# Kernel tuning notes

Hardware: AMD Instinct MI355X
Metric: run time of the kernel (lower is better)

The kernel has to match this reference:

```python
import jax, jax.numpy as jnp
import numpy as np

N_EMBED = 8192
EMBED_DIM = 64
BETA = 0.25


def setup_inputs() -> dict:
    key = jax.random.key(0)
    k_z, k_e = jax.random.split(key)
    z = jax.random.normal(k_z, (16, 4096, EMBED_DIM), dtype=jnp.float32)
    # embedding.weight.data.uniform_(-1/n_embed, 1/n_embed)
    embedding = jax.random.uniform(
        k_e, (N_EMBED, EMBED_DIM), dtype=jnp.float32,
        minval=-1.0 / N_EMBED, maxval=1.0 / N_EMBED)
    return {"z": z, "embedding": embedding}


def reference(z, embedding):
    # z: [B, H, C] with C == embed_dim (no permute needed)
    B, H, C = z.shape
    z_flat = z.reshape(-1, C)                      # [N, C]
    # squared euclidean distances: ||z||^2 + ||e||^2 - 2 z e^T
    d = (jnp.sum(z_flat ** 2, axis=1, keepdims=True)
         + jnp.sum(embedding ** 2, axis=1)
         - 2.0 * jnp.matmul(z_flat, embedding.T))  # [N, n_embed]
    idx = jnp.argmin(d, axis=1)                    # [N]
    z_q = embedding[idx].reshape(z.shape)          # gather + reshape
    sg = jax.lax.stop_gradient
    loss = (jnp.mean((sg(z_q) - z) ** 2)
            + BETA * jnp.mean((z_q - sg(z)) ** 2))
    # straight-through estimator
    z_q = z + sg(z_q - z)
    return z_q, loss, idx.reshape(B, H)
```

## Files before the change

### kernel.cpp

```cpp
#include <hip/hip_runtime.h>

typedef __attribute__((ext_vector_type(8))) short short8;
typedef __attribute__((ext_vector_type(16))) float floatx16;
typedef unsigned int u32;
typedef unsigned short u16;
typedef unsigned long long u64;

#define NROWS 65536
#define NEMB 8192
#define DIM 64
#define LOSS_OFF ((size_t)NROWS * DIM)
#define IDX_OFF (LOSS_OFF + 1)
#define CAPQ 20
#define CSTRIDE 82
#define NPRE 2

#define WS_EFRAG_OFF 0u
#define WS_LPART_OFF (1u << 20)
#define WS_QUEUE_OFF ((1u << 20) + 8192u)
#define WS_QCNT_OFF  ((1u << 20) + 8192u + (256u << 10))
#define WS_LOVR_OFF  (WS_QCNT_OFF + 4u)
#define WS_NEED      (WS_QCNT_OFF + 64u)

__device__ __forceinline__ unsigned short f2bf(float f) {
    u32 x = __float_as_uint(f);
    return (unsigned short)((x + 0x7fffu + ((x >> 16) & 1u)) >> 16);
}

__device__ __forceinline__ float zsum_np(const float* zf) {
    float r[8];
#pragma unroll
    for (int j = 0; j < 8; ++j) r[j] = zf[j] * zf[j];
#pragma unroll
    for (int i = 8; i < 64; i += 8) {
#pragma unroll
        for (int j = 0; j < 8; ++j) r[j] += zf[i + j] * zf[i + j];
    }
    return ((r[0] + r[1]) + (r[2] + r[3])) + ((r[4] + r[5]) + (r[6] + r[7]));
}

__device__ __forceinline__ float dot_chain(const float* zf, const float* e) {
    float acc = 0.f;
#pragma unroll
    for (int i = 0; i < 16; ++i) {
        float4 ev = ((const float4*)e)[i];
        acc = fmaf(zf[4 * i + 0], ev.x, acc);
        acc = fmaf(zf[4 * i + 1], ev.y, acc);
        acc = fmaf(zf[4 * i + 2], ev.z, acc);
        acc = fmaf(zf[4 * i + 3], ev.w, acc);
    }
    return acc;
}

__device__ __forceinline__ float vmax16_3(const floatx16& a) {
    float m0 = fmaxf(fmaxf(a[0], a[1]), a[2]);
    float m1 = fmaxf(fmaxf(a[3], a[4]), a[5]);
    float m2 = fmaxf(fmaxf(a[6], a[7]), a[8]);
    float m3 = fmaxf(fmaxf(a[9], a[10]), a[11]);
    float m4 = fmaxf(fmaxf(a[12], a[13]), a[14]);
    float n0 = fmaxf(fmaxf(m0, m1), m2);
    float n1 = fmaxf(fmaxf(m3, m4), a[15]);
    return fmaxf(n0, n1);
}

extern "C" __global__ __launch_bounds__(256)
void vq_prep(const float* __restrict__ emb, u32* __restrict__ efrag,
             u32* __restrict__ qcount, float* __restrict__ loss_over) {
    int tid = blockIdx.x * 256 + threadIdx.x;
    int t = tid >> 8, kc = (tid >> 5) & 7, m = tid & 31;
    const float* e = emb + (((size_t)t * 32 + m) * 64 + kc * 8);
    float4 a = ((const float4*)e)[0];
    float4 b = ((const float4*)e)[1];
    u32 w0 = (u32)f2bf(a.x) | ((u32)f2bf(a.y) << 16);
    u32 w1 = (u32)f2bf(a.z) | ((u32)f2bf(a.w) << 16);
    u32 w2 = (u32)f2bf(b.x) | ((u32)f2bf(b.y) << 16);
    u32 w3 = (u32)f2bf(b.z) | ((u32)f2bf(b.w) << 16);
    ((uint4*)efrag)[tid] = make_uint4(w0, w1, w2, w3);
    if (tid == 0) { qcount[0] = 0u; *loss_over = 0.f; }
}

extern "C" __global__ __launch_bounds__(256, 2)
void vq_screen(const float* __restrict__ z, const u32* __restrict__ efrag,
               const float* __restrict__ emb, float* __restrict__ out,
               float* __restrict__ lpart, u32* __restrict__ queue,
               u32* __restrict__ qcount) {
    __shared__ u16 cand[128 * CSTRIDE];
    __shared__ u32 cnt_l[512];
    __shared__ float runm_sh[128][2];
    __shared__ u32 win[128];
    __shared__ float lsum[4];
    const int tid = threadIdx.x;
    const int wave = tid >> 6, lane = tid & 63;
    const int rlo = lane & 31, h = lane >> 5;
    const int rowbase = blockIdx.x * 128 + (wave >> 1) * 64;
    const int sub = (wave & 1) * 2 + h;
    const int wp = wave & 1;

    if (tid < 128) { runm_sh[tid][0] = -3.4e38f; runm_sh[tid][1] = -3.4e38f; }

    short8 zfr[2][4];
    float eps_[2];
#pragma unroll
    for (int rt = 0; rt < 2; ++rt) {
        const float* zp = z + (size_t)(rowbase + rt * 32 + rlo) * 64;
        float sa = 0.f;
#pragma unroll
        for (int s = 0; s < 4; ++s) {
            const float4* p = (const float4*)(zp + s * 16 + h * 8);
            float4 a = p[0], b = p[1];
            union { short8 v; unsigned short e[8]; } u;
            u.e[0] = f2bf(a.x); u.e[1] = f2bf(a.y);
            u.e[2] = f2bf(a.z); u.e[3] = f2bf(a.w);
            u.e[4] = f2bf(b.x); u.e[5] = f2bf(b.y);
            u.e[6] = f2bf(b.z); u.e[7] = f2bf(b.w);
            zfr[rt][s] = u.v;
            sa += fabsf(a.x) + fabsf(a.y) + fabsf(a.z) + fabsf(a.w)
                + fabsf(b.x) + fabsf(b.y) + fabsf(b.z) + fabsf(b.w);
        }
        sa += __shfl_xor(sa, 32);
        eps_[rt] = fmaf(1.1e-6f, sa, 1e-7f);
    }
    float runm[2] = { -3.4e38f, -3.4e38f };
    u32 pc[2] = { 0u, 0u };
    __syncthreads();

    const u32* fbase = efrag + wp * 4096 + (size_t)h * 128 + (size_t)rlo * 4;
    for (int ii = 0; ii < 32 + NPRE; ++ii) {
        const int t = (ii < NPRE) ? ii : (ii - NPRE);
        const u32* tb = fbase + (size_t)t * 8192;

#pragma unroll
        for (int rt = 0; rt < 2; ++rt) {
            const int rowl = (wave >> 1) * 64 + rt * 32 + rlo;
            runm[rt] = fmaxf(runm[rt], runm_sh[rowl][wp ^ 1]);
        }

        floatx16 acc[4][2];
#pragma unroll
        for (int et = 0; et < 4; ++et)
#pragma unroll
            for (int rt = 0; rt < 2; ++rt) acc[et][rt] = 0.f;

#pragma unroll
        for (int s = 0; s < 4; ++s) {
            short8 af[4];
#pragma unroll
            for (int et = 0; et < 4; ++et)
                af[et] = *(const short8*)(tb + et * 1024 + s * 256);
#pragma unroll
            for (int et = 0; et < 4; ++et)
#pragma unroll
                for (int rt = 0; rt < 2; ++rt)
                    acc[et][rt] = __builtin_amdgcn_mfma_f32_32x32x16_bf16(
                        af[et], zfr[rt][s], acc[et][rt], 0, 0, 0);
        }

#pragma unroll
        for (int rt = 0; rt < 2; ++rt) {
            const int rowl = (wave >> 1) * 64 + rt * 32 + rlo;
            float vm[4];
#pragma unroll
            for (int et = 0; et < 4; ++et) vm[et] = vmax16_3(acc[et][rt]);
            float m64 = fmaxf(fmaxf(vm[0], vm[1]), fmaxf(vm[2], vm[3]));
            runm[rt] = fmaxf(runm[rt], m64);
            runm[rt] = fmaxf(runm[rt], __shfl_xor(runm[rt], 32));
            if (ii >= NPRE) {
                const float thr = runm[rt] - eps_[rt];
                if (m64 >= thr) {
                    const int ebase = t * 256 + wp * 128;
                    const u32 cbase = (u32)rowl * CSTRIDE + (u32)sub * CAPQ;
#pragma unroll
                    for (int et = 0; et < 4; ++et) {
                        if (vm[et] >= thr) {
#pragma unroll
                            for (int r = 0; r < 16; ++r) {
                                float v = acc[et][rt][r];
                                if (v >= thr) {
                                    int j = ebase + et * 32 + ((r & 3) + 8 * (r >> 2) + 4 * h);
                                    if (pc[rt] < CAPQ) cand[cbase + pc[rt]] = (u16)j;
                                    pc[rt]++;
                                }
                            }
                        }
                    }
                }
            }
            if (h == 0) runm_sh[rowl][wp] = runm[rt];
        }
    }
#pragma unroll
    for (int rt = 0; rt < 2; ++rt)
        cnt_l[(((wave >> 1) * 64 + rt * 32 + rlo) << 2) + sub] = pc[rt];
    __syncthreads();

    {
        const int rl = lane & 31, half = lane >> 5;
        const int rowl = wave * 32 + rl;
        const int grow = blockIdx.x * 128 + rowl;
        const u32 ca = cnt_l[(rowl << 2) + 2 * half];
        const u32 cb = cnt_l[(rowl << 2) + 2 * half + 1];
        u32 ovf = (u32)((ca > CAPQ) | (cb > CAPQ));
        ovf |= (u32)__shfl_xor((int)ovf, 32);

        if (!ovf) {
            float zf[64];
            const float4* zp = (const float4*)(z + (size_t)grow * 64);
#pragma unroll
            for (int i = 0; i < 16; ++i) {
                float4 a = zp[i];
                zf[4 * i + 0] = a.x; zf[4 * i + 1] = a.y;
                zf[4 * i + 2] = a.z; zf[4 * i + 3] = a.w;
            }
            const float zs = zsum_np(zf);
            u64 best = ~0ull;
            const u32 cbase = (u32)rowl * CSTRIDE + (u32)(2 * half) * CAPQ;
            for (u32 s = 0; s < ca; ++s) {
                u32 j = (u32)cand[cbase + s];
                float d = fmaf(-2.f, dot_chain(zf, emb + (size_t)j * 64), zs);
                u64 p = ((u64)__float_as_uint(d) << 32) | (u64)j;
                best = p < best ? p : best;
            }
            for (u32 s = 0; s < cb; ++s) {
                u32 j = (u32)cand[cbase + CAPQ + s];
                float d = fmaf(-2.f, dot_chain(zf, emb + (size_t)j * 64), zs);
                u64 p = ((u64)__float_as_uint(d) << 32) | (u64)j;
                best = p < best ? p : best;
            }
            u64 o = __shfl_xor(best, 32);
            best = o < best ? o : best;
            if (half == 0) {
                win[rowl] = (u32)best;
                out[IDX_OFF + grow] = (float)(u32)best;
            }
        } else if (half == 0) {
            u32 pos = atomicAdd(qcount, 1u);
            queue[pos] = (u32)grow;
            win[rowl] = 0xFFFFFFFFu;
        }
    }
    __syncthreads();

    float lp = 0.f;
    {
        const int r2 = tid >> 1, hf = tid & 1;
        const int grow2 = blockIdx.x * 128 + r2;
        const u32 wj = win[r2];
        if (wj != 0xFFFFFFFFu) {
            const float4* ep = (const float4*)(emb + (size_t)wj * 64) + hf * 8;
            const float4* zp4 = (const float4*)(z + (size_t)grow2 * 64) + hf * 8;
            float4* oq = (float4*)(out + (size_t)grow2 * 64) + hf * 8;
#pragma unroll
            for (int i = 0; i < 8; ++i) {
                float4 ev = ep[i];
                float4 zv = zp4[i];
                oq[i] = ev;
                float dx = ev.x - zv.x, dy = ev.y - zv.y;
                float dzv = ev.z - zv.z, dw = ev.w - zv.w;
                lp = fmaf(dx, dx, fmaf(dy, dy, fmaf(dzv, dzv, fmaf(dw, dw, lp))));
            }
        }
    }
#pragma unroll
    for (int off = 32; off; off >>= 1) lp += __shfl_down(lp, off);
    if (lane == 0) lsum[wave] = lp;
    __syncthreads();
    if (tid == 0)
        lpart[blockIdx.x] = (lsum[0] + lsum[1]) + (lsum[2] + lsum[3]);
}

extern "C" __global__ __launch_bounds__(256)
void vq_over(const float* __restrict__ z, const float* __restrict__ emb,
             const u32* __restrict__ queue, const u32* __restrict__ qcount,
             float* __restrict__ out, float* __restrict__ loss_over) {
    __shared__ u64 red[4];
    const int tid = threadIdx.x, wave = tid >> 6, lane = tid & 63;
    u32 n = qcount[0]; if (n > (u32)NROWS) n = (u32)NROWS;
    for (u32 qi = blockIdx.x; qi < n; qi += gridDim.x) {
        const int row = (int)queue[qi];
        const float4* zp = (const float4*)(z + (size_t)row * 64);
        float zf[64];
#pragma unroll
        for (int i = 0; i < 16; ++i) {
            float4 a = zp[i];
            zf[4 * i + 0] = a.x; zf[4 * i + 1] = a.y;
            zf[4 * i + 2] = a.z; zf[4 * i + 3] = a.w;
        }
        const float zs = zsum_np(zf);
        u64 best = ~0ull;
#pragma unroll 2
        for (int j = tid; j < NEMB; j += 256) {
            float d = fmaf(-2.f, dot_chain(zf, emb + (size_t)j * 64), zs);
            u64 p = ((u64)__float_as_uint(d) << 32) | (u64)j;
            best = p < best ? p : best;
        }
#pragma unroll
        for (int off = 32; off; off >>= 1) {
            u64 o = __shfl_xor(best, off);
            best = o < best ? o : best;
        }
        if (lane == 0) red[wave] = best;
        __syncthreads();
        if (tid == 0) {
            u64 b = red[0];
#pragma unroll
            for (int w = 1; w < 4; ++w) { u64 o = red[w]; b = o < b ? o : b; }
            red[0] = b;
            out[IDX_OFF + row] = (float)(u32)b;
        }
        __syncthreads();
        const u32 wj = (u32)red[0];
        float lp = 0.f;
        if (tid < 16) {
            float4 ev = ((const float4*)(emb + (size_t)wj * 64))[tid];
            float4 zv = zp[tid];
            ((float4*)(out + (size_t)row * 64))[tid] = ev;
            float dx = ev.x - zv.x, dy = ev.y - zv.y;
            float dzv = ev.z - zv.z, dw = ev.w - zv.w;
            lp = fmaf(dx, dx, fmaf(dy, dy, fmaf(dzv, dzv, dw * dw)));
        }
        if (wave == 0) {
#pragma unroll
            for (int off = 32; off; off >>= 1) lp += __shfl_down(lp, off);
            if (tid == 0) atomicAdd(loss_over, lp);
        }
        __syncthreads();
    }
}

extern "C" __global__ __launch_bounds__(256)
void vq_lossred(const float* __restrict__ lpart,
                const float* __restrict__ loss_over, float* __restrict__ out) {
    __shared__ float s[256];
    const int tid = threadIdx.x;
    float v = 0.f;
    for (int i = tid; i < 512; i += 256) v += lpart[i];
    s[tid] = v; __syncthreads();
    for (int off = 128; off; off >>= 1) {
        if (tid < off) s[tid] += s[tid + off];
        __syncthreads();
    }
    if (tid == 0) out[LOSS_OFF] = 1.25f * (s[0] + *loss_over) / 4194304.f;
}

extern "C" __global__ __launch_bounds__(256, 2)
void vq_legacy(const float* __restrict__ z, const float* __restrict__ emb,
               float* __restrict__ out, float* __restrict__ ws) {
    __shared__ float tile[128 * 64];
    __shared__ float red_d[4][128];
    __shared__ int   red_i[4][128];
    const int tid = threadIdx.x, lane = tid & 63, wave = tid >> 6;
    const int r0 = blockIdx.x * 128 + lane;
    float z0f[64], z1f[64];
    {
        const float4* p0 = (const float4*)(z + (size_t)r0 * 64);
        const float4* p1 = (const float4*)(z + ((size_t)r0 + 64) * 64);
#pragma unroll
        for (int i = 0; i < 16; ++i) {
            float4 a = p0[i];
            z0f[4*i+0]=a.x; z0f[4*i+1]=a.y; z0f[4*i+2]=a.z; z0f[4*i+3]=a.w;
            float4 b = p1[i];
            z1f[4*i+0]=b.x; z1f[4*i+1]=b.y; z1f[4*i+2]=b.z; z1f[4*i+3]=b.w;
        }
    }
    const float zs0 = zsum_np(z0f), zs1 = zsum_np(z1f);
    float bd0 = 3.402823466e38f, bd1 = 3.402823466e38f;
    int bi0 = 0, bi1 = 0;
    for (int t = 0; t < 64; ++t) {
        __syncthreads();
        {
            const float4* src = (const float4*)(emb + (size_t)t * 128 * 64);
            float4* dst = (float4*)tile;
#pragma unroll
            for (int i = 0; i < 8; ++i) dst[tid + i * 256] = src[tid + i * 256];
        }
        __syncthreads();
        const int base = wave * 32;
#pragma unroll 2
        for (int jg = 0; jg < 32; jg += 4) {
            const float* e = tile + (size_t)(base + jg) * 64;
            float a00=0,a10=0,a20=0,a30=0,a01=0,a11=0,a21=0,a31=0;
#pragma unroll
            for (int i = 0; i < 16; ++i) {
                float4 ea = ((const float4*)(e))[i];
                float4 eb = ((const float4*)(e + 64))[i];
                float4 ec = ((const float4*)(e + 128))[i];
                float4 ed = ((const float4*)(e + 192))[i];
                float x0=z0f[4*i],x1=z0f[4*i+1],x2=z0f[4*i+2],x3=z0f[4*i+3];
                float y0=z1f[4*i],y1=z1f[4*i+1],y2=z1f[4*i+2],y3=z1f[4*i+3];
                a00=fmaf(x0,ea.x,a00);a00=fmaf(x1,ea.y,a00);a00=fmaf(x2,ea.z,a00);a00=fmaf(x3,ea.w,a00);
                a10=fmaf(x0,eb.x,a10);a10=fmaf(x1,eb.y,a10);a10=fmaf(x2,eb.z,a10);a10=fmaf(x3,eb.w,a10);
                a20=fmaf(x0,ec.x,a20);a20=fmaf(x1,ec.y,a20);a20=fmaf(x2,ec.z,a20);a20=fmaf(x3,ec.w,a20);
                a30=fmaf(x0,ed.x,a30);a30=fmaf(x1,ed.y,a30);a30=fmaf(x2,ed.z,a30);a30=fmaf(x3,ed.w,a30);
                a01=fmaf(y0,ea.x,a01);a01=fmaf(y1,ea.y,a01);a01=fmaf(y2,ea.z,a01);a01=fmaf(y3,ea.w,a01);
                a11=fmaf(y0,eb.x,a11);a11=fmaf(y1,eb.y,a11);a11=fmaf(y2,eb.z,a11);a11=fmaf(y3,eb.w,a11);
                a21=fmaf(y0,ec.x,a21);a21=fmaf(y1,ec.y,a21);a21=fmaf(y2,ec.z,a21);a21=fmaf(y3,ec.w,a21);
                a31=fmaf(y0,ed.x,a31);a31=fmaf(y1,ed.y,a31);a31=fmaf(y2,ed.z,a31);a31=fmaf(y3,ed.w,a31);
            }
            const int gj = t * 128 + base + jg;
            float d;
            d=fmaf(-2.f,a00,zs0); if(d<bd0){bd0=d;bi0=gj;}
            d=fmaf(-2.f,a10,zs0); if(d<bd0){bd0=d;bi0=gj+1;}
            d=fmaf(-2.f,a20,zs0); if(d<bd0){bd0=d;bi0=gj+2;}
            d=fmaf(-2.f,a30,zs0); if(d<bd0){bd0=d;bi0=gj+3;}
            d=fmaf(-2.f,a01,zs1); if(d<bd1){bd1=d;bi1=gj;}
            d=fmaf(-2.f,a11,zs1); if(d<bd1){bd1=d;bi1=gj+1;}
            d=fmaf(-2.f,a21,zs1); if(d<bd1){bd1=d;bi1=gj+2;}
            d=fmaf(-2.f,a31,zs1); if(d<bd1){bd1=d;bi1=gj+3;}
        }
    }
    red_d[wave][lane]=bd0; red_i[wave][lane]=bi0;
    red_d[wave][lane+64]=bd1; red_i[wave][lane+64]=bi1;
    __syncthreads();
    if (wave == 0) {
        float blk = 0.f;
#pragma unroll
        for (int half = 0; half < 2; ++half) {
            const int lrow = lane + half * 64;
            const float* zrf = half ? z1f : z0f;
            float bd = red_d[0][lrow]; int bi = red_i[0][lrow];
#pragma unroll
            for (int w = 1; w < 4; ++w) {
                float dd = red_d[w][lrow]; int ii = red_i[w][lrow];
                if (dd < bd || (dd == bd && ii < bi)) { bd = dd; bi = ii; }
            }
            const size_t row = (size_t)blockIdx.x * 128 + lrow;
            out[IDX_OFF + row] = (float)bi;
            const float4* ep = (const float4*)(emb + (size_t)bi * 64);
            float4* oq = (float4*)(out + row * 64);
            float ls = 0.f;
#pragma unroll
            for (int i = 0; i < 16; ++i) {
                float4 ev = ep[i];
                oq[i] = ev;
                float dx=ev.x-zrf[4*i], dy=ev.y-zrf[4*i+1];
                float dzv=ev.z-zrf[4*i+2], dw=ev.w-zrf[4*i+3];
                ls=fmaf(dx,dx,ls); ls=fmaf(dy,dy,ls); ls=fmaf(dzv,dzv,ls); ls=fmaf(dw,dw,ls);
            }
            blk += ls;
        }
#pragma unroll
        for (int off = 32; off; off >>= 1) blk += __shfl_down(blk, off);
        if (lane == 0) ws[blockIdx.x] = blk;
    }
}

extern "C" __global__ __launch_bounds__(512)
void vq_legacy_loss(const float* __restrict__ ws, float* __restrict__ out) {
    __shared__ float s[8];
    const int tid = threadIdx.x;
    float v = ws[tid];
#pragma unroll
    for (int off = 32; off; off >>= 1) v += __shfl_down(v, off);
    if ((tid & 63) == 0) s[tid >> 6] = v;
    __syncthreads();
    if (tid == 0) {
        float t = 0.f;
#pragma unroll
        for (int i = 0; i < 8; ++i) t += s[i];
        out[LOSS_OFF] = 1.25f * t / 4194304.f;
    }
}

extern "C" void kernel_launch(void* const* d_in, const int* in_sizes, int n_in,
                              void* d_out, int out_size, void* d_ws, size_t ws_size,
                              hipStream_t stream) {
    const float* z   = (const float*)d_in[0];
    const float* emb = (const float*)d_in[1];
    float* out = (float*)d_out;
    if (ws_size < (size_t)WS_NEED) {
        float* ws = (float*)d_ws;
        vq_legacy<<<512, 256, 0, stream>>>(z, emb, out, ws);
        vq_legacy_loss<<<1, 512, 0, stream>>>(ws, out);
        return;
    }
    char* wsb = (char*)d_ws;
    u32* efrag = (u32*)(wsb + WS_EFRAG_OFF);
    float* lpart = (float*)(wsb + WS_LPART_OFF);
    u32* queue   = (u32*)(wsb + WS_QUEUE_OFF);
    u32* qcount  = (u32*)(wsb + WS_QCNT_OFF);
    float* loss_over = (float*)(wsb + WS_LOVR_OFF);
    vq_prep<<<256, 256, 0, stream>>>(emb, efrag, qcount, loss_over);
    vq_screen<<<512, 256, 0, stream>>>(z, efrag, emb, out, lpart, queue, qcount);
    vq_over<<<256, 256, 0, stream>>>(z, emb, queue, qcount, out, loss_over);
    vq_lossred<<<1, 256, 0, stream>>>(lpart, loss_over, out);
}
```

Measured before the change: 204.3 us.

## Split each screen block's codebook sweep across four waves over 64 rows

The screening kernel now processes 64 rows per block instead of 128. All four waves share the same rows, and each wave covers a quarter of every 256-entry codebook tile, where before two wave pairs each split a tile in half. The accumulator count per wave is halved, launch bounds rise to four blocks per SM, and the grid doubles to 1024 blocks. Candidate storage per sub-slice shrinks from 20 to 12, which may send more rows to the slower overflow path. Per-lane work in the rescoring and output phases is split four ways instead of two.

```diff
diff --git a/kernel.cpp b/kernel.cpp
--- a/kernel.cpp
+++ b/kernel.cpp
@@ -11,9 +11,12 @@
 #define DIM 64
 #define LOSS_OFF ((size_t)NROWS * DIM)
 #define IDX_OFF (LOSS_OFF + 1)
-#define CAPQ 20
-#define CSTRIDE 82
+#define CAPQ 12
+#define NSUB 8
+#define CSTRIDE 98
 #define NPRE 2
+#define ROWS_PB 64
+#define NBLK (NROWS / ROWS_PB)
 
 #define WS_EFRAG_OFF 0u
 #define WS_LPART_OFF (1u << 20)
@@ -79,24 +82,23 @@
     if (tid == 0) { qcount[0] = 0u; *loss_over = 0.f; }
 }
 
-extern "C" __global__ __launch_bounds__(256, 2)
+extern "C" __global__ __launch_bounds__(256, 4)
 void vq_screen(const float* __restrict__ z, const u32* __restrict__ efrag,
                const float* __restrict__ emb, float* __restrict__ out,
                float* __restrict__ lpart, u32* __restrict__ queue,
                u32* __restrict__ qcount) {
-    __shared__ u16 cand[128 * CSTRIDE];
-    __shared__ u32 cnt_l[512];
-    __shared__ float runm_sh[128][2];
-    __shared__ u32 win[128];
+    __shared__ u16 cand[ROWS_PB * CSTRIDE];
+    __shared__ u32 cnt_l[ROWS_PB * NSUB];
+    __shared__ float runm_sh[ROWS_PB];
+    __shared__ u32 win[ROWS_PB];
     __shared__ float lsum[4];
     const int tid = threadIdx.x;
     const int wave = tid >> 6, lane = tid & 63;
     const int rlo = lane & 31, h = lane >> 5;
-    const int rowbase = blockIdx.x * 128 + (wave >> 1) * 64;
-    const int sub = (wave & 1) * 2 + h;
-    const int wp = wave & 1;
-
-    if (tid < 128) { runm_sh[tid][0] = -3.4e38f; runm_sh[tid][1] = -3.4e38f; }
+    const int rowbase = blockIdx.x * ROWS_PB;
+    const int sub = wave * 2 + h;
+
+    if (tid < ROWS_PB) runm_sh[tid] = -3.4e38f;
 
     short8 zfr[2][4];
     float eps_[2];
@@ -124,31 +126,29 @@
     u32 pc[2] = { 0u, 0u };
     __syncthreads();
 
-    const u32* fbase = efrag + wp * 4096 + (size_t)h * 128 + (size_t)rlo * 4;
+    const u32* fbase = efrag + wave * 2048 + (size_t)h * 128 + (size_t)rlo * 4;
     for (int ii = 0; ii < 32 + NPRE; ++ii) {
         const int t = (ii < NPRE) ? ii : (ii - NPRE);
         const u32* tb = fbase + (size_t)t * 8192;
 
 #pragma unroll
-        for (int rt = 0; rt < 2; ++rt) {
-            const int rowl = (wave >> 1) * 64 + rt * 32 + rlo;
-            runm[rt] = fmaxf(runm[rt], runm_sh[rowl][wp ^ 1]);
-        }
-
-        floatx16 acc[4][2];
-#pragma unroll
-        for (int et = 0; et < 4; ++et)
+        for (int rt = 0; rt < 2; ++rt)
+            runm[rt] = fmaxf(runm[rt], runm_sh[rt * 32 + rlo]);
+
+        floatx16 acc[2][2];
+#pragma unroll
+        for (int et = 0; et < 2; ++et)
 #pragma unroll
             for (int rt = 0; rt < 2; ++rt) acc[et][rt] = 0.f;
 
 #pragma unroll
         for (int s = 0; s < 4; ++s) {
-            short8 af[4];
-#pragma unroll
-            for (int et = 0; et < 4; ++et)
+            short8 af[2];
+#pragma unroll
+            for (int et = 0; et < 2; ++et)
                 af[et] = *(const short8*)(tb + et * 1024 + s * 256);
 #pragma unroll
-            for (int et = 0; et < 4; ++et)
+            for (int et = 0; et < 2; ++et)
 #pragma unroll
                 for (int rt = 0; rt < 2; ++rt)
                     acc[et][rt] = __builtin_amdgcn_mfma_f32_32x32x16_bf16(
@@ -157,20 +157,20 @@
 
 #pragma unroll
         for (int rt = 0; rt < 2; ++rt) {
-            const int rowl = (wave >> 1) * 64 + rt * 32 + rlo;
-            float vm[4];
-#pragma unroll
-            for (int et = 0; et < 4; ++et) vm[et] = vmax16_3(acc[et][rt]);
-            float m64 = fmaxf(fmaxf(vm[0], vm[1]), fmaxf(vm[2], vm[3]));
+            const int rowl = rt * 32 + rlo;
+            float vm[2];
+            vm[0] = vmax16_3(acc[0][rt]);
+            vm[1] = vmax16_3(acc[1][rt]);
+            float m64 = fmaxf(vm[0], vm[1]);
             runm[rt] = fmaxf(runm[rt], m64);
             runm[rt] = fmaxf(runm[rt], __shfl_xor(runm[rt], 32));
             if (ii >= NPRE) {
                 const float thr = runm[rt] - eps_[rt];
                 if (m64 >= thr) {
-                    const int ebase = t * 256 + wp * 128;
+                    const int ebase = t * 256 + wave * 64;
                     const u32 cbase = (u32)rowl * CSTRIDE + (u32)sub * CAPQ;
 #pragma unroll
-                    for (int et = 0; et < 4; ++et) {
+                    for (int et = 0; et < 2; ++et) {
                         if (vm[et] >= thr) {
 #pragma unroll
                             for (int r = 0; r < 16; ++r) {
@@ -185,22 +185,23 @@
                     }
                 }
             }
-            if (h == 0) runm_sh[rowl][wp] = runm[rt];
+            if (h == 0) runm_sh[rowl] = runm[rt];
         }
     }
 #pragma unroll
     for (int rt = 0; rt < 2; ++rt)
-        cnt_l[(((wave >> 1) * 64 + rt * 32 + rlo) << 2) + sub] = pc[rt];
+        cnt_l[(rt * 32 + rlo) * NSUB + sub] = pc[rt];
     __syncthreads();
 
     {
-        const int rl = lane & 31, half = lane >> 5;
-        const int rowl = wave * 32 + rl;
-        const int grow = blockIdx.x * 128 + rowl;
-        const u32 ca = cnt_l[(rowl << 2) + 2 * half];
-        const u32 cb = cnt_l[(rowl << 2) + 2 * half + 1];
-        u32 ovf = (u32)((ca > CAPQ) | (cb > CAPQ));
-        ovf |= (u32)__shfl_xor((int)ovf, 32);
+        const int rowl = wave * 16 + (lane >> 2);
+        const int q = lane & 3;
+        const int grow = rowbase + rowl;
+        const u32 c0 = cnt_l[rowl * NSUB + 2 * q];
+        const u32 c1 = cnt_l[rowl * NSUB + 2 * q + 1];
+        u32 ovf = (u32)((c0 > CAPQ) | (c1 > CAPQ));
+        ovf |= (u32)__shfl_xor((int)ovf, 1);
+        ovf |= (u32)__shfl_xor((int)ovf, 2);
 
         if (!ovf) {
             float zf[64];
@@ -213,26 +214,26 @@
             }
             const float zs = zsum_np(zf);
             u64 best = ~0ull;
-            const u32 cbase = (u32)rowl * CSTRIDE + (u32)(2 * half) * CAPQ;
-            for (u32 s = 0; s < ca; ++s) {
+            const u32 cbase = (u32)rowl * CSTRIDE + (u32)(2 * q) * CAPQ;
+            for (u32 s = 0; s < c0; ++s) {
                 u32 j = (u32)cand[cbase + s];
                 float d = fmaf(-2.f, dot_chain(zf, emb + (size_t)j * 64), zs);
                 u64 p = ((u64)__float_as_uint(d) << 32) | (u64)j;
                 best = p < best ? p : best;
             }
-            for (u32 s = 0; s < cb; ++s) {
+            for (u32 s = 0; s < c1; ++s) {
                 u32 j = (u32)cand[cbase + CAPQ + s];
                 float d = fmaf(-2.f, dot_chain(zf, emb + (size_t)j * 64), zs);
                 u64 p = ((u64)__float_as_uint(d) << 32) | (u64)j;
                 best = p < best ? p : best;
             }
-            u64 o = __shfl_xor(best, 32);
-            best = o < best ? o : best;
-            if (half == 0) {
+            u64 o = __shfl_xor(best, 1); best = o < best ? o : best;
+            o = __shfl_xor(best, 2);     best = o < best ? o : best;
+            if (q == 0) {
                 win[rowl] = (u32)best;
                 out[IDX_OFF + grow] = (float)(u32)best;
             }
-        } else if (half == 0) {
+        } else if (q == 0) {
             u32 pos = atomicAdd(qcount, 1u);
             queue[pos] = (u32)grow;
             win[rowl] = 0xFFFFFFFFu;
@@ -242,15 +243,15 @@
 
     float lp = 0.f;
     {
-        const int r2 = tid >> 1, hf = tid & 1;
-        const int grow2 = blockIdx.x * 128 + r2;
+        const int r2 = tid >> 2, hf = tid & 3;
+        const int grow2 = rowbase + r2;
         const u32 wj = win[r2];
         if (wj != 0xFFFFFFFFu) {
-            const float4* ep = (const float4*)(emb + (size_t)wj * 64) + hf * 8;
-            const float4* zp4 = (const float4*)(z + (size_t)grow2 * 64) + hf * 8;
-            float4* oq = (float4*)(out + (size_t)grow2 * 64) + hf * 8;
-#pragma unroll
-            for (int i = 0; i < 8; ++i) {
+            const float4* ep = (const float4*)(emb + (size_t)wj * 64) + hf * 4;
+            const float4* zp4 = (const float4*)(z + (size_t)grow2 * 64) + hf * 4;
+            float4* oq = (float4*)(out + (size_t)grow2 * 64) + hf * 4;
+#pragma unroll
+            for (int i = 0; i < 4; ++i) {
                 float4 ev = ep[i];
                 float4 zv = zp4[i];
                 oq[i] = ev;
@@ -333,7 +334,7 @@
     __shared__ float s[256];
     const int tid = threadIdx.x;
     float v = 0.f;
-    for (int i = tid; i < 512; i += 256) v += lpart[i];
+    for (int i = tid; i < NBLK; i += 256) v += lpart[i];
     s[tid] = v; __syncthreads();
     for (int off = 128; off; off >>= 1) {
         if (tid < off) s[tid] += s[tid + off];
@@ -480,7 +481,7 @@
     u32* qcount  = (u32*)(wsb + WS_QCNT_OFF);
     float* loss_over = (float*)(wsb + WS_LOVR_OFF);
     vq_prep<<<256, 256, 0, stream>>>(emb, efrag, qcount, loss_over);
-    vq_screen<<<512, 256, 0, stream>>>(z, efrag, emb, out, lpart, queue, qcount);
+    vq_screen<<<NBLK, 256, 0, stream>>>(z, efrag, emb, out, lpart, queue, qcount);
     vq_over<<<256, 256, 0, stream>>>(z, emb, queue, qcount, out, loss_over);
     vq_lossred<<<1, 256, 0, stream>>>(lpart, loss_over, out);
 }
```

Result: slower. 288.7 us (+41.3%).
